# Kernel optimization log

Hardware: AMD Instinct MI355X
Metric: run time of the kernel (lower is better)

Reference implementation:

```python
import jax, jax.numpy as jnp
import numpy as np

B = 1000        # graphs in batch
T_PER = 250     # tasks per graph
M_PER = 50      # machines per graph
N_T = B * T_PER
N_M = B * M_PER
D_T = 16        # INPUT_TASK_DIM
D_M = 8         # INPUT_MACHINE_DIM
H = 128         # hidden_dim
IN_PREV_IDX = 0
TASK_FEAT_IDX = 1
EPS = 1e-5      # BatchNorm eps


def _mk_params(rng):
    def lin(i, o):
        return (rng.standard_normal((i, o)).astype(np.float32) / np.sqrt(i),
                np.zeros(o, np.float32))
    p = {}
    p['bn_t_gamma'] = np.ones(D_T, np.float32); p['bn_t_beta'] = np.zeros(D_T, np.float32)
    p['Wt1'], p['bt1'] = lin(D_T, H); p['Wt2'], p['bt2'] = lin(H, H)
    p['bn_m_gamma'] = np.ones(D_M, np.float32); p['bn_m_beta'] = np.zeros(D_M, np.float32)
    p['Wm1'], p['bm1'] = lin(D_M, H); p['Wm2'], p['bm2'] = lin(H, H)
    p['Wa1'], p['ba1'] = lin(2 * H, H); p['Wa2'], p['ba2'] = lin(H, H)
    p['Wl1'], p['bl1'] = lin(3 * H, H); p['Wl2'], p['bl2'] = lin(H, H)
    p['Wo1'], p['bo1'] = lin(H, H); p['Wo2'], p['bo2'] = lin(H, 1)
    return p


def setup_inputs() -> dict:
    rng = np.random.default_rng(0)
    xt = rng.standard_normal((N_T, D_T)).astype(np.float32)
    # prev-task flag: even task ids are 'prev'
    xt[:, IN_PREV_IDX] = (np.arange(N_T) % 2 == 0).astype(np.float32)
    # per-graph machine assignment in [0, M_PER), or -1 (unassigned) every 10th task
    lm = rng.integers(0, M_PER, N_T)
    lm[np.arange(N_T) % 10 == 0] = -1
    xt[:, TASK_FEAT_IDX] = lm.astype(np.float32)
    xm = rng.standard_normal((N_M, D_M)).astype(np.float32)
    inp = {'x_tasks': jnp.asarray(xt), 'x_machines': jnp.asarray(xm)}
    inp.update({k: jnp.asarray(v) for k, v in _mk_params(rng).items()})
    inp['x_tasks_batch'] = jnp.asarray(np.repeat(np.arange(B), T_PER).astype(np.int32))
    inp['x_machines_batch'] = jnp.asarray(np.repeat(np.arange(B), M_PER).astype(np.int32))
    # labels are tasks 0,5,10,...; prev tasks are even ids -> prev-local index t//2
    # label tasks that are prev: t % 10 == 0 -> prev_tasks_label_idx = 5*arange(N_T//10)
    inp['label_idx'] = jnp.asarray((5 * np.arange(N_T // 10)).astype(np.int32))
    inp['num_graphs'] = B
    return inp


def _bn(x, g, b):
    # BatchNorm1d in training mode: biased batch stats
    mu = x.mean(axis=0)
    var = x.var(axis=0)
    return g * (x - mu) * jax.lax.rsqrt(var + EPS) + b


def _seg_mean(x, seg, n):
    s = jax.ops.segment_sum(x, seg, num_segments=n)
    c = jax.ops.segment_sum(jnp.ones((x.shape[0], 1), x.dtype), seg, num_segments=n)
    return s / jnp.maximum(c, 1.0)


def reference(x_tasks, x_machines, bn_t_gamma, bn_t_beta, Wt1, bt1, Wt2, bt2,
              bn_m_gamma, bn_m_beta, Wm1, bm1, Wm2, bm2,
              Wa1, ba1, Wa2, ba2, Wl1, bl1, Wl2, bl2,
              Wo1, bo1, Wo2, bo2,
              x_tasks_batch, x_machines_batch, label_idx, num_graphs):
    nm = x_machines.shape[0]
    # tasks_select_assignment: local machine id -> global machine row (or pad row nm)
    tm_col = x_tasks[:, TASK_FEAT_IDX]
    cnt_m = jnp.bincount(x_machines_batch, length=num_graphs)
    cum = jnp.cumsum(cnt_m) - cnt_m  # cumulative machines per graph
    task_m = jnp.where(tm_col == -1.0, nm,
                       tm_col.astype(jnp.int32) + cum[x_tasks_batch].astype(jnp.int32))
    # node embeddings: BN -> Linear -> ReLU -> Linear -> ReLU
    th = jax.nn.relu(jax.nn.relu(_bn(x_tasks, bn_t_gamma, bn_t_beta) @ Wt1 + bt1) @ Wt2 + bt2)
    mh = jax.nn.relu(jax.nn.relu(_bn(x_machines, bn_m_gamma, bn_m_beta) @ Wm1 + bm1) @ Wm2 + bm2)
    # global aggregation per graph (scatter_mean) + MLP
    aggr = jnp.concatenate([_seg_mean(th, x_tasks_batch, num_graphs),
                            _seg_mean(mh, x_machines_batch, num_graphs)], axis=1)
    aggr = jax.nn.relu(aggr @ Wa1 + ba1) @ Wa2 + ba2
    # gather machine embedding per task (pad row of zeros for unassigned)
    mh_pad = jnp.concatenate([mh, jnp.zeros((1, H), mh.dtype)], axis=0)
    cat = jnp.concatenate([th, aggr[x_tasks_batch], mh_pad[task_m]], axis=1)  # [N_T, 3H]
    h = jax.nn.relu(cat @ Wl1 + bl1) @ Wl2 + bl2
    out = (jax.nn.relu(h @ Wo1 + bo1) @ Wo2 + bo2)[label_idx]
    return out
```

## Files before the change

### kernel.cpp

```cpp
#include <hip/hip_runtime.h>
#include <hip/hip_bf16.h>

constexpr int B     = 1000;
constexpr int T_PER = 250;
constexpr int M_PER = 50;
constexpr int N_T   = B * T_PER;
constexpr int N_M   = B * M_PER;
constexpr int H     = 128;
constexpr int N_LBL = 25000;
constexpr float EPS = 1e-05f;

constexpr int NB_T = 256;
constexpr int NB_M = 64;
constexpr int NB_P = 64;

constexpr int OFF_PART_T = 0;
constexpr int OFF_PART_M = OFF_PART_T + NB_T * 32;
constexpr int OFF_AT     = OFF_PART_M + NB_M * 16;
constexpr int OFF_BT     = OFF_AT + 16;
constexpr int OFF_AM     = OFF_BT + 16;
constexpr int OFF_BM     = OFF_AM + 8;
constexpr int OFF_BT1F   = OFF_BM + 8;
constexpr int OFF_BM1F   = OFF_BT1F + 128;
constexpr int OFF_MEANT  = OFF_BM1F + 128;
constexpr int OFF_MEANM  = OFF_MEANT + B * H;
constexpr int OFF_HALF   = OFF_MEANM + B * H;
constexpr int HO_WT1  = 0;
constexpr int HO_WT2  = 4096;
constexpr int HO_WM1  = 20480;
constexpr int HO_WM2  = 24576;
constexpr int HO_WA1  = 40960;
constexpr int HO_WA2  = 73728;
constexpr int HO_WL1  = 90112;
constexpr int HO_WL2  = 139264;
constexpr int HO_WO1  = 155648;

typedef _Float16 f16x8 __attribute__((ext_vector_type(8)));
typedef _Float16 f16x4 __attribute__((ext_vector_type(4)));
typedef float f32x4 __attribute__((ext_vector_type(4)));

#define MFMA16(a, b, c) __builtin_amdgcn_mfma_f32_16x16x32_f16(a, b, c, 0, 0, 0)

template <int C, int NB>
__device__ __forceinline__ void stats_body(const float* __restrict__ x, int nelem,
                                           float* __restrict__ part, int blk, int t,
                                           float* ls, float* lq) {
    float s = 0.f, q = 0.f;
    for (int e = blk * 256 + t; e < nelem; e += NB * 256) {
        float v = x[e];
        s += v;
        q += v * v;
    }
    ls[t] = s; lq[t] = q;
    __syncthreads();
    if (t < C) {
        float S = 0.f, Q = 0.f;
        for (int u = t; u < 256; u += C) { S += ls[u]; Q += lq[u]; }
        part[blk * 2 * C + t] = S;
        part[blk * 2 * C + C + t] = Q;
    }
}

__device__ __forceinline__ void cvt_tr(const float* __restrict__ src, _Float16* __restrict__ dst,
                                       int K, int Kp, int tid, int nt) {
    for (int idx = tid; idx < 128 * Kp; idx += nt) {
        int c = idx / Kp, k = idx - c * Kp;
        float v = (k < K) ? src[k * 128 + c] : 0.f;
        dst[idx] = (_Float16)v;
    }
}

__global__ __launch_bounds__(256) void stats_prep_kernel(
        const float* __restrict__ xt, const float* __restrict__ xm,
        const float* __restrict__ Wt1, const float* __restrict__ Wt2,
        const float* __restrict__ Wm1, const float* __restrict__ Wm2,
        const float* __restrict__ Wa1, const float* __restrict__ Wa2,
        const float* __restrict__ Wl1, const float* __restrict__ Wl2,
        const float* __restrict__ Wo1,
        float* __restrict__ wsf, _Float16* __restrict__ wh) {
    __shared__ float ls[256], lq[256];
    const int bid = blockIdx.x, t = threadIdx.x;
    if (bid < NB_T) {
        stats_body<16, NB_T>(xt, N_T * 16, wsf + OFF_PART_T, bid, t, ls, lq);
    } else if (bid < NB_T + NB_M) {
        stats_body<8, NB_M>(xm, N_M * 8, wsf + OFF_PART_M, bid - NB_T, t, ls, lq);
    } else {
        const int tid = (bid - NB_T - NB_M) * 256 + t;
        const int nt = NB_P * 256;
        cvt_tr(Wt1, wh + HO_WT1, 16, 32, tid, nt);
        cvt_tr(Wt2, wh + HO_WT2, 128, 128, tid, nt);
        cvt_tr(Wm1, wh + HO_WM1, 8, 32, tid, nt);
        cvt_tr(Wm2, wh + HO_WM2, 128, 128, tid, nt);
        cvt_tr(Wa1, wh + HO_WA1, 256, 256, tid, nt);
        cvt_tr(Wa2, wh + HO_WA2, 128, 128, tid, nt);
        cvt_tr(Wl1, wh + HO_WL1, 384, 384, tid, nt);
        cvt_tr(Wl2, wh + HO_WL2, 128, 128, tid, nt);
        cvt_tr(Wo1, wh + HO_WO1, 128, 128, tid, nt);
    }
}

__global__ __launch_bounds__(256) void finalize_kernel(
        const float* __restrict__ gt, const float* __restrict__ btb,
        const float* __restrict__ gm, const float* __restrict__ bmb,
        const float* __restrict__ Wt1, const float* __restrict__ bt1,
        const float* __restrict__ Wm1, const float* __restrict__ bm1,
        float* __restrict__ ws) {
    __shared__ float red[256];
    __shared__ float statT[32], statM[16];
    __shared__ float shT[16], shM[8];
    const int t = threadIdx.x;
    {
        const int slot = t & 31, chunk = t >> 5;
        const float* p = ws + OFF_PART_T;
        float s = 0.f;
        for (int b = chunk * 32; b < chunk * 32 + 32; b++) s += p[b * 32 + slot];
        red[t] = s;
    }
    __syncthreads();
    if (t < 32) {
        float v = 0.f;
#pragma unroll
        for (int c = 0; c < 8; c++) v += red[t + 32 * c];
        statT[t] = v;
    }
    __syncthreads();
    {
        float s = 0.f;
        if (t < 128) {
            const int slot = t & 15, chunk = t >> 4;
            const float* p = ws + OFF_PART_M;
            for (int b = chunk * 8; b < chunk * 8 + 8; b++) s += p[b * 16 + slot];
        }
        red[t] = s;
    }
    __syncthreads();
    if (t < 16) {
        float v = 0.f;
#pragma unroll
        for (int c = 0; c < 8; c++) v += red[t + 16 * c];
        statM[t] = v;
    }
    __syncthreads();
    if (t < 16) {
        float mu  = statT[t] / (float)N_T;
        float var = statT[16 + t] / (float)N_T - mu * mu;
        float a   = gt[t] * rsqrtf(var + EPS);
        ws[OFF_AT + t] = a;
        float b = btb[t] - mu * a;
        ws[OFF_BT + t] = b;
        shT[t] = b;
    } else if (t < 24) {
        int c = t - 16;
        float mu  = statM[c] / (float)N_M;
        float var = statM[8 + c] / (float)N_M - mu * mu;
        float a   = gm[c] * rsqrtf(var + EPS);
        ws[OFF_AM + c] = a;
        float b = bmb[c] - mu * a;
        ws[OFF_BM + c] = b;
        shM[c] = b;
    }
    __syncthreads();
    if (t < 128) {
        float s = bt1[t];
#pragma unroll
        for (int k = 0; k < 16; k++) s += shT[k] * Wt1[k * 128 + t];
        ws[OFF_BT1F + t] = s;
    } else {
        int c = t - 128;
        float s = bm1[c];
#pragma unroll
        for (int k = 0; k < 8; k++) s += shM[k] * Wm1[k * 128 + c];
        ws[OFF_BM1F + c] = s;
    }
}

__device__ __forceinline__ void zacc(f32x4 acc[4][2]) {
#pragma unroll
    for (int rg = 0; rg < 4; rg++)
#pragma unroll
        for (int mi = 0; mi < 2; mi++) acc[rg][mi] = (f32x4){0.f, 0.f, 0.f, 0.f};
}

__device__ __forceinline__ void ld32(f16x8 w[2], const _Float16* __restrict__ WT,
                                     int m0, int r, int gq) {
#pragma unroll
    for (int mi = 0; mi < 2; mi++)
        w[mi] = *(const f16x8*)(WT + ((m0 + mi) * 16 + r) * 32 + gq * 8);
}

__device__ __forceinline__ void ld128(f16x8 w[2][4], const _Float16* __restrict__ WT,
                                      int lda, int k0, int m0, int r, int gq) {
#pragma unroll
    for (int mi = 0; mi < 2; mi++)
#pragma unroll
        for (int ks = 0; ks < 4; ks++)
            w[mi][ks] = *(const f16x8*)(WT + ((m0 + mi) * 16 + r) * lda + k0 + ks * 32 + gq * 8);
}

__device__ __forceinline__ void mm32(const f16x8 w[2], const _Float16* __restrict__ act,
                                     int rstride, int r, int gq, f32x4 acc[4][2]) {
#pragma unroll
    for (int rg = 0; rg < 4; rg++) {
        const f16x8 bf = *(const f16x8*)(act + (rg * 16 + r) * rstride + gq * 8);
        acc[rg][0] = MFMA16(w[0], bf, acc[rg][0]);
        acc[rg][1] = MFMA16(w[1], bf, acc[rg][1]);
    }
}

__device__ __forceinline__ void mm128(const f16x8 w[2][4], const _Float16* __restrict__ act,
                                      int rstride, int r, int gq, f32x4 acc[4][2]) {
#pragma unroll
    for (int rg = 0; rg < 4; rg++)
#pragma unroll
        for (int ks = 0; ks < 4; ks++) {
            const f16x8 bf = *(const f16x8*)(act + (rg * 16 + r) * rstride + ks * 32 + gq * 8);
            acc[rg][0] = MFMA16(w[0][ks], bf, acc[rg][0]);
            acc[rg][1] = MFMA16(w[1][ks], bf, acc[rg][1]);
        }
}

__device__ __forceinline__ void epi_cs(const f32x4 acc[4][2], const f32x4 bv[2],
                                       _Float16* __restrict__ dst, int dstride,
                                       int m0, int r, int gq, bool relu) {
#pragma unroll
    for (int rg = 0; rg < 4; rg++)
#pragma unroll
        for (int mi = 0; mi < 2; mi++) {
            f16x4 hv;
#pragma unroll
            for (int j = 0; j < 4; j++) {
                float v = acc[rg][mi][j] + bv[mi][j];
                if (relu) v = fmaxf(v, 0.f);
                hv[j] = (_Float16)v;
            }
            *(f16x4*)(dst + (rg * 16 + r) * dstride + (m0 + mi) * 16 + gq * 4) = hv;
        }
}

template <int CIN, int ROWS, int PASSES>
__device__ __forceinline__ void seg_body(const float* __restrict__ x, const float* __restrict__ scaleA,
        const _Float16* __restrict__ W1T, const float* __restrict__ b1,
        const _Float16* __restrict__ W2T, const float* __restrict__ b2,
        float* __restrict__ meanout, int g, int t,
        _Float16* __restrict__ xs, _Float16* __restrict__ h1s) {
    const int lane = t & 63, wave = t >> 6;
    const int r = lane & 15, gq = lane >> 4;
    const int m0 = 2 * wave;
    f16x8 w1[2], w2[2][4];
    ld32(w1, W1T, m0, r, gq);
    ld128(w2, W2T, 128, 0, m0, r, gq);
    f32x4 b1v[2], b2v[2];
#pragma unroll
    for (int mi = 0; mi < 2; mi++) {
        b1v[mi] = *(const f32x4*)(b1 + (m0 + mi) * 16 + gq * 4);
        b2v[mi] = *(const f32x4*)(b2 + (m0 + mi) * 16 + gq * 4);
    }
    const int jrow = (CIN == 16) ? (t >> 2) : (t >> 1);
    const int part = (CIN == 16) ? (t & 3) : (t & 1);
    const bool stager = (CIN == 16) ? true : (t < 128);
    f32x4 av = {0.f, 0.f, 0.f, 0.f};
    if (stager) av = *(const f32x4*)(scaleA + part * 4);
    f16x4 z4; z4[0] = z4[1] = z4[2] = z4[3] = (_Float16)0.f;
    if (stager) {
        if (CIN == 16) {
            *(f16x4*)(xs + jrow * 40 + 16 + part * 4) = z4;
        } else {
#pragma unroll
            for (int q = 0; q < 3; q++)
                *(f16x4*)(xs + jrow * 40 + 8 + part * 12 + q * 4) = z4;
        }
    }
    float4 xr = {0.f, 0.f, 0.f, 0.f};
    if (stager) {
        int cl = (jrow < ROWS) ? jrow : (ROWS - 1);
        xr = *(const float4*)(x + (g * ROWS + cl) * CIN + part * 4);
    }
    f32x4 rs[2];
    rs[0] = (f32x4){0.f, 0.f, 0.f, 0.f};
    rs[1] = (f32x4){0.f, 0.f, 0.f, 0.f};
    for (int p = 0; p < PASSES; p++) {
        if (stager) {
            const bool valid = (p * 64 + jrow) < ROWS;
            f16x4 hv;
            hv[0] = (_Float16)(valid ? av[0] * xr.x : 0.f);
            hv[1] = (_Float16)(valid ? av[1] * xr.y : 0.f);
            hv[2] = (_Float16)(valid ? av[2] * xr.z : 0.f);
            hv[3] = (_Float16)(valid ? av[3] * xr.w : 0.f);
            *(f16x4*)(xs + jrow * 40 + part * 4) = hv;
        }
        __syncthreads();
        if (p + 1 < PASSES && stager) {
            int lr = (p + 1) * 64 + jrow;
            int cl = (lr < ROWS) ? lr : (ROWS - 1);
            xr = *(const float4*)(x + (g * ROWS + cl) * CIN + part * 4);
        }
        f32x4 acc[4][2];
        zacc(acc);
        mm32(w1, xs, 40, r, gq, acc);
        epi_cs(acc, b1v, h1s, 136, m0, r, gq, true);
        __syncthreads();
        zacc(acc);
        mm128(w2, h1s, 136, r, gq, acc);
#pragma unroll
        for (int rg = 0; rg < 4; rg++) {
            const bool vr = (p * 64 + rg * 16 + r) < ROWS;
#pragma unroll
            for (int mi = 0; mi < 2; mi++)
#pragma unroll
                for (int j = 0; j < 4; j++) {
                    float v = fmaxf(acc[rg][mi][j] + b2v[mi][j], 0.f);
                    rs[mi][j] += vr ? v : 0.f;
                }
        }
    }
#pragma unroll
    for (int mi = 0; mi < 2; mi++)
#pragma unroll
        for (int j = 0; j < 4; j++) {
            float v = rs[mi][j];
            v += __shfl_xor(v, 1); v += __shfl_xor(v, 2);
            v += __shfl_xor(v, 4); v += __shfl_xor(v, 8);
            rs[mi][j] = v;
        }
    if (r == 0) {
        constexpr float inv = 1.f / (float)ROWS;
#pragma unroll
        for (int mi = 0; mi < 2; mi++) {
            f32x4 st = rs[mi] * inv;
            *(f32x4*)(meanout + g * H + (m0 + mi) * 16 + gq * 4) = st;
        }
    }
}

__global__ __launch_bounds__(256) void seg_fused(const float* __restrict__ xt, const float* __restrict__ xm,
        const _Float16* __restrict__ wh, const float* __restrict__ wsf,
        const float* __restrict__ bt2, const float* __restrict__ bm2,
        float* __restrict__ meanT, float* __restrict__ meanM) {
    __shared__ __attribute__((aligned(16))) _Float16 xs[64 * 40];
    __shared__ __attribute__((aligned(16))) _Float16 h1s[64 * 136];
    if (blockIdx.x < B)
        seg_body<16, T_PER, 4>(xt, wsf + OFF_AT, wh + HO_WT1, wsf + OFF_BT1F,
                               wh + HO_WT2, bt2, meanT, blockIdx.x, threadIdx.x, xs, h1s);
    else
        seg_body<8, M_PER, 1>(xm, wsf + OFF_AM, wh + HO_WM1, wsf + OFF_BM1F,
                              wh + HO_WM2, bm2, meanM, blockIdx.x - B, threadIdx.x, xs, h1s);
}

__global__ __launch_bounds__(256) void aggr_kernel(const float* __restrict__ meanT, const float* __restrict__ meanM,
        const _Float16* __restrict__ Wa1T, const float* __restrict__ ba1,
        const _Float16* __restrict__ Wa2T, const float* __restrict__ ba2,
        const _Float16* __restrict__ Wl1T, const float* __restrict__ bl1,
        float* __restrict__ agg2) {
    __shared__ __attribute__((aligned(16))) _Float16 cin[16 * 264];
    __shared__ __attribute__((aligned(16))) _Float16 h1s[16 * 136];
    __shared__ __attribute__((aligned(16))) _Float16 ags[16 * 136];
    const int t = threadIdx.x, lane = t & 63, wave = t >> 6;
    const int r = lane & 15, gq = lane >> 4;
    const int m0 = 2 * wave;
    const int g0 = blockIdx.x * 16;
    f16x8 wa1[2][8], wa2[2][4], wl1b[2][4];
#pragma unroll
    for (int mi = 0; mi < 2; mi++)
#pragma unroll
        for (int ks = 0; ks < 8; ks++)
            wa1[mi][ks] = *(const f16x8*)(Wa1T + ((m0 + mi) * 16 + r) * 256 + ks * 32 + gq * 8);
    ld128(wa2, Wa2T, 128, 0, m0, r, gq);
    ld128(wl1b, Wl1T, 384, 128, m0, r, gq);
    f32x4 b1v[2], b2v[2], blv[2];
#pragma unroll
    for (int mi = 0; mi < 2; mi++) {
        b1v[mi] = *(const f32x4*)(ba1 + (m0 + mi) * 16 + gq * 4);
        b2v[mi] = *(const f32x4*)(ba2 + (m0 + mi) * 16 + gq * 4);
        blv[mi] = *(const f32x4*)(bl1 + (m0 + mi) * 16 + gq * 4);
    }
    for (int e = t; e < 16 * 64; e += 256) {
        int j = e >> 6, c4 = e & 63;
        int g = g0 + j;
        float4 v = {0.f, 0.f, 0.f, 0.f};
        if (g < B) v = (c4 < 32) ? *(const float4*)(meanT + g * H + c4 * 4)
                                 : *(const float4*)(meanM + g * H + (c4 - 32) * 4);
        f16x4 hv;
        hv[0] = (_Float16)v.x; hv[1] = (_Float16)v.y; hv[2] = (_Float16)v.z; hv[3] = (_Float16)v.w;
        *(f16x4*)(cin + j * 264 + c4 * 4) = hv;
    }
    __syncthreads();
    f32x4 a0 = {0.f, 0.f, 0.f, 0.f}, a1 = {0.f, 0.f, 0.f, 0.f};
    {
        const _Float16* bp = cin + r * 264 + gq * 8;
#pragma unroll
        for (int ks = 0; ks < 8; ks++) {
            const f16x8 bf = *(const f16x8*)(bp + ks * 32);
            a0 = MFMA16(wa1[0][ks], bf, a0);
            a1 = MFMA16(wa1[1][ks], bf, a1);
        }
    }
    {
        f16x4 h0, h1v;
#pragma unroll
        for (int j = 0; j < 4; j++) {
            h0[j]  = (_Float16)fmaxf(a0[j] + b1v[0][j], 0.f);
            h1v[j] = (_Float16)fmaxf(a1[j] + b1v[1][j], 0.f);
        }
        *(f16x4*)(h1s + r * 136 + m0 * 16 + gq * 4) = h0;
        *(f16x4*)(h1s + r * 136 + (m0 + 1) * 16 + gq * 4) = h1v;
    }
    __syncthreads();
    a0 = (f32x4){0.f, 0.f, 0.f, 0.f}; a1 = (f32x4){0.f, 0.f, 0.f, 0.f};
    {
        const _Float16* bp = h1s + r * 136 + gq * 8;
#pragma unroll
        for (int ks = 0; ks < 4; ks++) {
            const f16x8 bf = *(const f16x8*)(bp + ks * 32);
            a0 = MFMA16(wa2[0][ks], bf, a0);
            a1 = MFMA16(wa2[1][ks], bf, a1);
        }
    }
    {
        f16x4 h0, h1v;
#pragma unroll
        for (int j = 0; j < 4; j++) {
            h0[j]  = (_Float16)(a0[j] + b2v[0][j]);
            h1v[j] = (_Float16)(a1[j] + b2v[1][j]);
        }
        *(f16x4*)(ags + r * 136 + m0 * 16 + gq * 4) = h0;
        *(f16x4*)(ags + r * 136 + (m0 + 1) * 16 + gq * 4) = h1v;
    }
    __syncthreads();
    a0 = (f32x4){0.f, 0.f, 0.f, 0.f}; a1 = (f32x4){0.f, 0.f, 0.f, 0.f};
    {
        const _Float16* bp = ags + r * 136 + gq * 8;
#pragma unroll
        for (int ks = 0; ks < 4; ks++) {
            const f16x8 bf = *(const f16x8*)(bp + ks * 32);
            a0 = MFMA16(wl1b[0][ks], bf, a0);
            a1 = MFMA16(wl1b[1][ks], bf, a1);
        }
    }
    if (g0 + r < B) {
        *(f32x4*)(agg2 + (g0 + r) * H + m0 * 16 + gq * 4) = a0 + blv[0];
        *(f32x4*)(agg2 + (g0 + r) * H + (m0 + 1) * 16 + gq * 4) = a1 + blv[1];
    }
}

__global__ __launch_bounds__(256) void label_kernel(
        const float* __restrict__ xt, const float* __restrict__ xm,
        const float* __restrict__ scT, const float* __restrict__ scM,
        const _Float16* __restrict__ Wt1T, const float* __restrict__ bt1f,
        const _Float16* __restrict__ Wt2T, const float* __restrict__ bt2,
        const _Float16* __restrict__ Wm1T, const float* __restrict__ bm1f,
        const _Float16* __restrict__ Wm2T, const float* __restrict__ bm2,
        const _Float16* __restrict__ Wl1T,
        const _Float16* __restrict__ Wl2T, const float* __restrict__ bl2,
        const _Float16* __restrict__ Wo1T, const float* __restrict__ bo1,
        const float* __restrict__ Wo2, const float* __restrict__ bo2,
        const float* __restrict__ agg2,
        const int* __restrict__ tbatch, const int* __restrict__ lidx,
        float* __restrict__ out) {
    __shared__ __attribute__((aligned(16))) _Float16 xs_t[64 * 40];
    __shared__ __attribute__((aligned(16))) _Float16 xs_m[64 * 40];
    __shared__ __attribute__((aligned(16))) _Float16 h1s[64 * 136];
    __shared__ __attribute__((aligned(16))) _Float16 cat[64 * 264];
    __shared__ float psum[4][64];
    __shared__ int ridx[64], gidx[64], midx[64];
    const int t = threadIdx.x;
    const int lane = t & 63, wave = t >> 6;
    const int r = lane & 15, gq = lane >> 4;
    const int m0 = 2 * wave;
    if (t < 64) {
        int i = blockIdx.x * 64 + t;
        int rr = (i < N_LBL) ? lidx[i] : 0;
        ridx[t] = rr;
        int gg = tbatch[rr];
        gidx[t] = gg;
        float tv = xt[rr * 16 + 1];
        midx[t] = (tv == -1.0f) ? -1 : ((int)tv + gg * M_PER);
    }
    __syncthreads();
    f16x4 z4; z4[0] = z4[1] = z4[2] = z4[3] = (_Float16)0.f;
    {
        int j = t >> 2, part = t & 3;
        f32x4 avt = *(const f32x4*)(scT + part * 4);
        float4 v = *(const float4*)(xt + ridx[j] * 16 + part * 4);
        f16x4 hv;
        hv[0] = (_Float16)(avt[0] * v.x); hv[1] = (_Float16)(avt[1] * v.y);
        hv[2] = (_Float16)(avt[2] * v.z); hv[3] = (_Float16)(avt[3] * v.w);
        *(f16x4*)(xs_t + j * 40 + part * 4) = hv;
        *(f16x4*)(xs_t + j * 40 + 16 + part * 4) = z4;
    }
    if (t < 128) {
        int j = t >> 1, part = t & 1;
        f32x4 avm = *(const f32x4*)(scM + part * 4);
        int m = midx[j];
        f16x4 hv = z4;
        if (m >= 0) {
            float4 v = *(const float4*)(xm + m * 8 + part * 4);
            hv[0] = (_Float16)(avm[0] * v.x); hv[1] = (_Float16)(avm[1] * v.y);
            hv[2] = (_Float16)(avm[2] * v.z); hv[3] = (_Float16)(avm[3] * v.w);
        }
        *(f16x4*)(xs_m + j * 40 + part * 4) = hv;
#pragma unroll
        for (int q = 0; q < 3; q++)
            *(f16x4*)(xs_m + j * 40 + 8 + part * 12 + q * 4) = z4;
    }
    __syncthreads();
    f32x4 agg2v[4][2];
#pragma unroll
    for (int rg = 0; rg < 4; rg++)
#pragma unroll
        for (int mi = 0; mi < 2; mi++)
            agg2v[rg][mi] = *(const f32x4*)(agg2 + gidx[rg * 16 + r] * H + (m0 + mi) * 16 + gq * 4);
    f32x4 acc[4][2];
    f16x8 wt1[2]; ld32(wt1, Wt1T, m0, r, gq);
    f16x8 wt2[2][4]; ld128(wt2, Wt2T, 128, 0, m0, r, gq);
    f32x4 bva[2], bvb[2];
#pragma unroll
    for (int mi = 0; mi < 2; mi++) {
        bva[mi] = *(const f32x4*)(bt1f + (m0 + mi) * 16 + gq * 4);
        bvb[mi] = *(const f32x4*)(bt2 + (m0 + mi) * 16 + gq * 4);
    }
    zacc(acc);
    mm32(wt1, xs_t, 40, r, gq, acc);
    epi_cs(acc, bva, h1s, 136, m0, r, gq, true);
    f16x8 wm1[2]; ld32(wm1, Wm1T, m0, r, gq);
    __syncthreads();
    zacc(acc);
    mm128(wt2, h1s, 136, r, gq, acc);
    epi_cs(acc, bvb, cat, 264, m0, r, gq, true);
    f16x8 wm2[2][4]; ld128(wm2, Wm2T, 128, 0, m0, r, gq);
    __syncthreads();
#pragma unroll
    for (int mi = 0; mi < 2; mi++) {
        bva[mi] = *(const f32x4*)(bm1f + (m0 + mi) * 16 + gq * 4);
        bvb[mi] = *(const f32x4*)(bm2 + (m0 + mi) * 16 + gq * 4);
    }
    zacc(acc);
    mm32(wm1, xs_m, 40, r, gq, acc);
    epi_cs(acc, bva, h1s, 136, m0, r, gq, true);
    f16x8 wl1a[2][4]; ld128(wl1a, Wl1T, 384, 0, m0, r, gq);
    __syncthreads();
    zacc(acc);
    mm128(wm2, h1s, 136, r, gq, acc);
#pragma unroll
    for (int rg = 0; rg < 4; rg++) {
        const bool sent = (midx[rg * 16 + r] < 0);
#pragma unroll
        for (int mi = 0; mi < 2; mi++) {
            f16x4 hv;
#pragma unroll
            for (int j = 0; j < 4; j++) {
                float v = fmaxf(acc[rg][mi][j] + bvb[mi][j], 0.f);
                hv[j] = (_Float16)(sent ? 0.f : v);
            }
            *(f16x4*)(cat + (rg * 16 + r) * 264 + 128 + (m0 + mi) * 16 + gq * 4) = hv;
        }
    }
    f16x8 wl1c[2][4]; ld128(wl1c, Wl1T, 384, 256, m0, r, gq);
    __syncthreads();
    zacc(acc);
    mm128(wl1a, cat, 264, r, gq, acc);
    mm128(wl1c, cat + 128, 264, r, gq, acc);
#pragma unroll
    for (int rg = 0; rg < 4; rg++)
#pragma unroll
        for (int mi = 0; mi < 2; mi++) {
            f16x4 hv;
#pragma unroll
            for (int j = 0; j < 4; j++)
                hv[j] = (_Float16)fmaxf(acc[rg][mi][j] + agg2v[rg][mi][j], 0.f);
            *(f16x4*)(h1s + (rg * 16 + r) * 136 + (m0 + mi) * 16 + gq * 4) = hv;
        }
    f16x8 wl2[2][4]; ld128(wl2, Wl2T, 128, 0, m0, r, gq);
    __syncthreads();
#pragma unroll
    for (int mi = 0; mi < 2; mi++) bva[mi] = *(const f32x4*)(bl2 + (m0 + mi) * 16 + gq * 4);
    zacc(acc);
    mm128(wl2, h1s, 136, r, gq, acc);
    epi_cs(acc, bva, cat, 264, m0, r, gq, false);
    f16x8 wo1[2][4]; ld128(wo1, Wo1T, 128, 0, m0, r, gq);
    __syncthreads();
#pragma unroll
    for (int mi = 0; mi < 2; mi++) bva[mi] = *(const f32x4*)(bo1 + (m0 + mi) * 16 + gq * 4);
    f32x4 wo2v[2];
#pragma unroll
    for (int mi = 0; mi < 2; mi++) wo2v[mi] = *(const f32x4*)(Wo2 + (m0 + mi) * 16 + gq * 4);
    zacc(acc);
    mm128(wo1, cat, 264, r, gq, acc);
#pragma unroll
    for (int rg = 0; rg < 4; rg++) {
        float pv = 0.f;
#pragma unroll
        for (int mi = 0; mi < 2; mi++)
#pragma unroll
            for (int j = 0; j < 4; j++)
                pv += fmaxf(acc[rg][mi][j] + bva[mi][j], 0.f) * wo2v[mi][j];
        pv += __shfl_xor(pv, 16);
        pv += __shfl_xor(pv, 32);
        if (lane < 16) psum[wave][rg * 16 + lane] = pv;
    }
    __syncthreads();
    if (t < 64) {
        int i = blockIdx.x * 64 + t;
        if (i < N_LBL)
            out[i] = psum[0][t] + psum[1][t] + psum[2][t] + psum[3][t] + bo2[0];
    }
}

extern "C" void kernel_launch(void* const* d_in, const int* in_sizes, int n_in,
                              void* d_out, int out_size, void* d_ws, size_t ws_size,
                              hipStream_t stream) {
    const float* xt  = (const float*)d_in[0];
    const float* xm  = (const float*)d_in[1];
    const float* gt  = (const float*)d_in[2];
    const float* btb = (const float*)d_in[3];
    const float* Wt1 = (const float*)d_in[4];  const float* bt1 = (const float*)d_in[5];
    const float* Wt2 = (const float*)d_in[6];  const float* bt2 = (const float*)d_in[7];
    const float* gm  = (const float*)d_in[8];  const float* bmb = (const float*)d_in[9];
    const float* Wm1 = (const float*)d_in[10]; const float* bm1 = (const float*)d_in[11];
    const float* Wm2 = (const float*)d_in[12]; const float* bm2 = (const float*)d_in[13];
    const float* Wa1 = (const float*)d_in[14]; const float* ba1 = (const float*)d_in[15];
    const float* Wa2 = (const float*)d_in[16]; const float* ba2 = (const float*)d_in[17];
    const float* Wl1 = (const float*)d_in[18]; const float* bl1 = (const float*)d_in[19];
    const float* Wl2 = (const float*)d_in[20]; const float* bl2 = (const float*)d_in[21];
    const float* Wo1 = (const float*)d_in[22]; const float* bo1 = (const float*)d_in[23];
    const float* Wo2 = (const float*)d_in[24]; const float* bo2 = (const float*)d_in[25];
    const int* tb  = (const int*)d_in[26];
    const int* lix = (const int*)d_in[28];
    float* wsf = (float*)d_ws;
    _Float16* wh = (_Float16*)(wsf + OFF_HALF);
    float* outp = (float*)d_out;

    stats_prep_kernel<<<NB_T + NB_M + NB_P, 256, 0, stream>>>(
        xt, xm, Wt1, Wt2, Wm1, Wm2, Wa1, Wa2, Wl1, Wl2, Wo1, wsf, wh);
    finalize_kernel<<<1, 256, 0, stream>>>(gt, btb, gm, bmb, Wt1, bt1, Wm1, bm1, wsf);
    seg_fused<<<2 * B, 256, 0, stream>>>(xt, xm, wh, wsf, bt2, bm2,
                                         wsf + OFF_MEANT, wsf + OFF_MEANM);
    aggr_kernel<<<(B + 15) / 16, 256, 0, stream>>>(wsf + OFF_MEANT, wsf + OFF_MEANM,
                                                   wh + HO_WA1, ba1, wh + HO_WA2, ba2,
                                                   wh + HO_WL1, bl1, wsf + OFF_MEANT);
    label_kernel<<<(N_LBL + 63) / 64, 256, 0, stream>>>(xt, xm,
                                                        wsf + OFF_AT, wsf + OFF_AM,
                                                        wh + HO_WT1, wsf + OFF_BT1F, wh + HO_WT2, bt2,
                                                        wh + HO_WM1, wsf + OFF_BM1F, wh + HO_WM2, bm2,
                                                        wh + HO_WL1,
                                                        wh + HO_WL2, bl2,
                                                        wh + HO_WO1, bo1, Wo2, bo2,
                                                        wsf + OFF_MEANT, tb, lix, outp);
}
```

Measured before the change: 74.12 us.

## Fuse BN finalize and aggregation MLP into consumers, stage inputs as fp16

Removes the single-block finalize kernel and the aggr kernel. Each seg and label block now recomputes the BatchNorm statistics from the partial sums and folds the scale into the first-layer weights. The label kernel computes the per-graph aggregation MLP for the graphs it touches in shared memory. The stats pass also writes fp16 copies of the task and machine inputs so later kernels read half the bytes. This cuts two launches and their serialization, at the cost of redundant per-block reductions and MLP work, plus an extra fp16 write in the stats pass.

```diff
diff --git a/kernel.cpp b/kernel.cpp
--- a/kernel.cpp
+++ b/kernel.cpp
@@ -1,5 +1,4 @@
 #include <hip/hip_runtime.h>
-#include <hip/hip_bf16.h>
 
 constexpr int B     = 1000;
 constexpr int T_PER = 250;
@@ -16,13 +15,7 @@
 
 constexpr int OFF_PART_T = 0;
 constexpr int OFF_PART_M = OFF_PART_T + NB_T * 32;
-constexpr int OFF_AT     = OFF_PART_M + NB_M * 16;
-constexpr int OFF_BT     = OFF_AT + 16;
-constexpr int OFF_AM     = OFF_BT + 16;
-constexpr int OFF_BM     = OFF_AM + 8;
-constexpr int OFF_BT1F   = OFF_BM + 8;
-constexpr int OFF_BM1F   = OFF_BT1F + 128;
-constexpr int OFF_MEANT  = OFF_BM1F + 128;
+constexpr int OFF_MEANT  = OFF_PART_M + NB_M * 16;
 constexpr int OFF_MEANM  = OFF_MEANT + B * H;
 constexpr int OFF_HALF   = OFF_MEANM + B * H;
 constexpr int HO_WT1  = 0;
@@ -34,6 +27,8 @@
 constexpr int HO_WL1  = 90112;
 constexpr int HO_WL2  = 139264;
 constexpr int HO_WO1  = 155648;
+constexpr int HO_XT16 = 172032;
+constexpr int HO_XM16 = HO_XT16 + N_T * 16;
 
 typedef _Float16 f16x8 __attribute__((ext_vector_type(8)));
 typedef _Float16 f16x4 __attribute__((ext_vector_type(4)));
@@ -42,7 +37,8 @@
 #define MFMA16(a, b, c) __builtin_amdgcn_mfma_f32_16x16x32_f16(a, b, c, 0, 0, 0)
 
 template <int C, int NB>
-__device__ __forceinline__ void stats_body(const float* __restrict__ x, int nelem,
+__device__ __forceinline__ void stats_body(const float* __restrict__ x,
+                                           _Float16* __restrict__ x16, int nelem,
                                            float* __restrict__ part, int blk, int t,
                                            float* ls, float* lq) {
     float s = 0.f, q = 0.f;
@@ -50,6 +46,7 @@
         float v = x[e];
         s += v;
         q += v * v;
+        x16[e] = (_Float16)v;
     }
     ls[t] = s; lq[t] = q;
     __syncthreads();
@@ -72,6 +69,7 @@
 
 __global__ __launch_bounds__(256) void stats_prep_kernel(
         const float* __restrict__ xt, const float* __restrict__ xm,
+        _Float16* __restrict__ xt16, _Float16* __restrict__ xm16,
         const float* __restrict__ Wt1, const float* __restrict__ Wt2,
         const float* __restrict__ Wm1, const float* __restrict__ Wm2,
         const float* __restrict__ Wa1, const float* __restrict__ Wa2,
@@ -81,9 +79,9 @@
     __shared__ float ls[256], lq[256];
     const int bid = blockIdx.x, t = threadIdx.x;
     if (bid < NB_T) {
-        stats_body<16, NB_T>(xt, N_T * 16, wsf + OFF_PART_T, bid, t, ls, lq);
+        stats_body<16, NB_T>(xt, xt16, N_T * 16, wsf + OFF_PART_T, bid, t, ls, lq);
     } else if (bid < NB_T + NB_M) {
-        stats_body<8, NB_M>(xm, N_M * 8, wsf + OFF_PART_M, bid - NB_T, t, ls, lq);
+        stats_body<8, NB_M>(xm, xm16, N_M * 8, wsf + OFF_PART_M, bid - NB_T, t, ls, lq);
     } else {
         const int tid = (bid - NB_T - NB_M) * 256 + t;
         const int nt = NB_P * 256;
@@ -99,81 +97,6 @@
     }
 }
 
-__global__ __launch_bounds__(256) void finalize_kernel(
-        const float* __restrict__ gt, const float* __restrict__ btb,
-        const float* __restrict__ gm, const float* __restrict__ bmb,
-        const float* __restrict__ Wt1, const float* __restrict__ bt1,
-        const float* __restrict__ Wm1, const float* __restrict__ bm1,
-        float* __restrict__ ws) {
-    __shared__ float red[256];
-    __shared__ float statT[32], statM[16];
-    __shared__ float shT[16], shM[8];
-    const int t = threadIdx.x;
-    {
-        const int slot = t & 31, chunk = t >> 5;
-        const float* p = ws + OFF_PART_T;
-        float s = 0.f;
-        for (int b = chunk * 32; b < chunk * 32 + 32; b++) s += p[b * 32 + slot];
-        red[t] = s;
-    }
-    __syncthreads();
-    if (t < 32) {
-        float v = 0.f;
-#pragma unroll
-        for (int c = 0; c < 8; c++) v += red[t + 32 * c];
-        statT[t] = v;
-    }
-    __syncthreads();
-    {
-        float s = 0.f;
-        if (t < 128) {
-            const int slot = t & 15, chunk = t >> 4;
-            const float* p = ws + OFF_PART_M;
-            for (int b = chunk * 8; b < chunk * 8 + 8; b++) s += p[b * 16 + slot];
-        }
-        red[t] = s;
-    }
-    __syncthreads();
-    if (t < 16) {
-        float v = 0.f;
-#pragma unroll
-        for (int c = 0; c < 8; c++) v += red[t + 16 * c];
-        statM[t] = v;
-    }
-    __syncthreads();
-    if (t < 16) {
-        float mu  = statT[t] / (float)N_T;
-        float var = statT[16 + t] / (float)N_T - mu * mu;
-        float a   = gt[t] * rsqrtf(var + EPS);
-        ws[OFF_AT + t] = a;
-        float b = btb[t] - mu * a;
-        ws[OFF_BT + t] = b;
-        shT[t] = b;
-    } else if (t < 24) {
-        int c = t - 16;
-        float mu  = statM[c] / (float)N_M;
-        float var = statM[8 + c] / (float)N_M - mu * mu;
-        float a   = gm[c] * rsqrtf(var + EPS);
-        ws[OFF_AM + c] = a;
-        float b = bmb[c] - mu * a;
-        ws[OFF_BM + c] = b;
-        shM[c] = b;
-    }
-    __syncthreads();
-    if (t < 128) {
-        float s = bt1[t];
-#pragma unroll
-        for (int k = 0; k < 16; k++) s += shT[k] * Wt1[k * 128 + t];
-        ws[OFF_BT1F + t] = s;
-    } else {
-        int c = t - 128;
-        float s = bm1[c];
-#pragma unroll
-        for (int k = 0; k < 8; k++) s += shM[k] * Wm1[k * 128 + c];
-        ws[OFF_BM1F + c] = s;
-    }
-}
-
 __device__ __forceinline__ void zacc(f32x4 acc[4][2]) {
 #pragma unroll
     for (int rg = 0; rg < 4; rg++)
@@ -237,43 +160,85 @@
         }
 }
 
-template <int CIN, int ROWS, int PASSES>
-__device__ __forceinline__ void seg_body(const float* __restrict__ x, const float* __restrict__ scaleA,
-        const _Float16* __restrict__ W1T, const float* __restrict__ b1,
-        const _Float16* __restrict__ W2T, const float* __restrict__ b2,
-        float* __restrict__ meanout, int g, int t,
-        _Float16* __restrict__ xs, _Float16* __restrict__ h1s) {
+template <int CIN, int ROWS, int PASSES, int NBS, int NTOT>
+__device__ __forceinline__ void seg_body(
+        const _Float16* __restrict__ x16, const float* __restrict__ pstats,
+        const float* __restrict__ gamma, const float* __restrict__ beta,
+        const float* __restrict__ W1f, const float* __restrict__ b1,
+        const _Float16* __restrict__ W1T, const _Float16* __restrict__ W2T,
+        const float* __restrict__ b2, float* __restrict__ meanout,
+        int g, int t,
+        _Float16* __restrict__ xs, _Float16* __restrict__ h1s,
+        float* __restrict__ red, float* __restrict__ stat,
+        float* __restrict__ sa, float* __restrict__ sb, float* __restrict__ b1f) {
+    constexpr int S2 = 2 * CIN;
+    constexpr int NCH = 256 / S2;
+    {
+        const int slot = t & (S2 - 1), chunk = t / S2;
+        float s = 0.f;
+        for (int b = chunk; b < NBS; b += NCH) s += pstats[b * S2 + slot];
+        red[t] = s;
+    }
+    __syncthreads();
+    if (t < S2) {
+        float v = 0.f;
+#pragma unroll
+        for (int c = 0; c < NCH; c++) v += red[t + S2 * c];
+        stat[t] = v;
+    }
+    __syncthreads();
+    if (t < CIN) {
+        float mu  = stat[t] * (1.f / (float)NTOT);
+        float var = stat[CIN + t] * (1.f / (float)NTOT) - mu * mu;
+        float a   = gamma[t] * rsqrtf(var + EPS);
+        sa[t] = a;
+        sb[t] = beta[t] - mu * a;
+    }
+    __syncthreads();
+    if (t < 128) {
+        float s = b1[t];
+#pragma unroll
+        for (int k = 0; k < CIN; k++) s += sb[k] * W1f[k * 128 + t];
+        b1f[t] = s;
+    }
+    __syncthreads();
+
     const int lane = t & 63, wave = t >> 6;
     const int r = lane & 15, gq = lane >> 4;
     const int m0 = 2 * wave;
     f16x8 w1[2], w2[2][4];
     ld32(w1, W1T, m0, r, gq);
+    if (gq * 8 < CIN) {
+#pragma unroll
+        for (int mi = 0; mi < 2; mi++)
+#pragma unroll
+            for (int e = 0; e < 8; e++)
+                w1[mi][e] = (_Float16)((float)w1[mi][e] * sa[gq * 8 + e]);
+    }
     ld128(w2, W2T, 128, 0, m0, r, gq);
     f32x4 b1v[2], b2v[2];
 #pragma unroll
     for (int mi = 0; mi < 2; mi++) {
-        b1v[mi] = *(const f32x4*)(b1 + (m0 + mi) * 16 + gq * 4);
+        b1v[mi] = *(const f32x4*)(b1f + (m0 + mi) * 16 + gq * 4);
         b2v[mi] = *(const f32x4*)(b2 + (m0 + mi) * 16 + gq * 4);
     }
     const int jrow = (CIN == 16) ? (t >> 2) : (t >> 1);
-    const int part = (CIN == 16) ? (t & 3) : (t & 1);
+    const int prt  = (CIN == 16) ? (t & 3) : (t & 1);
     const bool stager = (CIN == 16) ? true : (t < 128);
-    f32x4 av = {0.f, 0.f, 0.f, 0.f};
-    if (stager) av = *(const f32x4*)(scaleA + part * 4);
     f16x4 z4; z4[0] = z4[1] = z4[2] = z4[3] = (_Float16)0.f;
     if (stager) {
         if (CIN == 16) {
-            *(f16x4*)(xs + jrow * 40 + 16 + part * 4) = z4;
+            *(f16x4*)(xs + jrow * 40 + 16 + prt * 4) = z4;
         } else {
 #pragma unroll
             for (int q = 0; q < 3; q++)
-                *(f16x4*)(xs + jrow * 40 + 8 + part * 12 + q * 4) = z4;
-        }
-    }
-    float4 xr = {0.f, 0.f, 0.f, 0.f};
+                *(f16x4*)(xs + jrow * 40 + 8 + prt * 12 + q * 4) = z4;
+        }
+    }
+    f16x4 xr = z4;
     if (stager) {
         int cl = (jrow < ROWS) ? jrow : (ROWS - 1);
-        xr = *(const float4*)(x + (g * ROWS + cl) * CIN + part * 4);
+        xr = *(const f16x4*)(x16 + (g * ROWS + cl) * CIN + prt * 4);
     }
     f32x4 rs[2];
     rs[0] = (f32x4){0.f, 0.f, 0.f, 0.f};
@@ -281,18 +246,14 @@
     for (int p = 0; p < PASSES; p++) {
         if (stager) {
             const bool valid = (p * 64 + jrow) < ROWS;
-            f16x4 hv;
-            hv[0] = (_Float16)(valid ? av[0] * xr.x : 0.f);
-            hv[1] = (_Float16)(valid ? av[1] * xr.y : 0.f);
-            hv[2] = (_Float16)(valid ? av[2] * xr.z : 0.f);
-            hv[3] = (_Float16)(valid ? av[3] * xr.w : 0.f);
-            *(f16x4*)(xs + jrow * 40 + part * 4) = hv;
+            f16x4 hv = valid ? xr : z4;
+            *(f16x4*)(xs + jrow * 40 + prt * 4) = hv;
         }
         __syncthreads();
         if (p + 1 < PASSES && stager) {
             int lr = (p + 1) * 64 + jrow;
             int cl = (lr < ROWS) ? lr : (ROWS - 1);
-            xr = *(const float4*)(x + (g * ROWS + cl) * CIN + part * 4);
+            xr = *(const f16x4*)(x16 + (g * ROWS + cl) * CIN + prt * 4);
         }
         f32x4 acc[4][2];
         zacc(acc);
@@ -301,16 +262,24 @@
         __syncthreads();
         zacc(acc);
         mm128(w2, h1s, 136, r, gq, acc);
-#pragma unroll
-        for (int rg = 0; rg < 4; rg++) {
-            const bool vr = (p * 64 + rg * 16 + r) < ROWS;
-#pragma unroll
-            for (int mi = 0; mi < 2; mi++)
-#pragma unroll
-                for (int j = 0; j < 4; j++) {
-                    float v = fmaxf(acc[rg][mi][j] + b2v[mi][j], 0.f);
-                    rs[mi][j] += vr ? v : 0.f;
-                }
+        if ((p + 1) * 64 <= ROWS) {
+#pragma unroll
+            for (int rg = 0; rg < 4; rg++)
+#pragma unroll
+                for (int mi = 0; mi < 2; mi++)
+#pragma unroll
+                    for (int j = 0; j < 4; j++)
+                        rs[mi][j] += fmaxf(acc[rg][mi][j] + b2v[mi][j], 0.f);
+        } else {
+#pragma unroll
+            for (int rg = 0; rg < 4; rg++) {
+                const float mk = ((p * 64 + rg * 16 + r) < ROWS) ? 1.f : 0.f;
+#pragma unroll
+                for (int mi = 0; mi < 2; mi++)
+#pragma unroll
+                    for (int j = 0; j < 4; j++)
+                        rs[mi][j] = fmaf(fmaxf(acc[rg][mi][j] + b2v[mi][j], 0.f), mk, rs[mi][j]);
+            }
         }
     }
 #pragma unroll
@@ -332,128 +301,42 @@
     }
 }
 
-__global__ __launch_bounds__(256) void seg_fused(const float* __restrict__ xt, const float* __restrict__ xm,
-        const _Float16* __restrict__ wh, const float* __restrict__ wsf,
+__global__ __launch_bounds__(256) void seg_fused(
+        const _Float16* __restrict__ xt16, const _Float16* __restrict__ xm16,
+        const float* __restrict__ wsf,
+        const float* __restrict__ gt, const float* __restrict__ btb,
+        const float* __restrict__ gm, const float* __restrict__ bmb,
+        const float* __restrict__ Wt1f, const float* __restrict__ bt1,
+        const float* __restrict__ Wm1f, const float* __restrict__ bm1,
+        const _Float16* __restrict__ wh,
         const float* __restrict__ bt2, const float* __restrict__ bm2,
         float* __restrict__ meanT, float* __restrict__ meanM) {
     __shared__ __attribute__((aligned(16))) _Float16 xs[64 * 40];
     __shared__ __attribute__((aligned(16))) _Float16 h1s[64 * 136];
+    __shared__ float red[256], stat[32], sa[16], sb[16], b1f[128];
     if (blockIdx.x < B)
-        seg_body<16, T_PER, 4>(xt, wsf + OFF_AT, wh + HO_WT1, wsf + OFF_BT1F,
-                               wh + HO_WT2, bt2, meanT, blockIdx.x, threadIdx.x, xs, h1s);
+        seg_body<16, T_PER, 4, NB_T, N_T>(xt16, wsf + OFF_PART_T, gt, btb, Wt1f, bt1,
+                                          wh + HO_WT1, wh + HO_WT2, bt2, meanT,
+                                          blockIdx.x, threadIdx.x, xs, h1s, red, stat, sa, sb, b1f);
     else
-        seg_body<8, M_PER, 1>(xm, wsf + OFF_AM, wh + HO_WM1, wsf + OFF_BM1F,
-                              wh + HO_WM2, bm2, meanM, blockIdx.x - B, threadIdx.x, xs, h1s);
-}
-
-__global__ __launch_bounds__(256) void aggr_kernel(const float* __restrict__ meanT, const float* __restrict__ meanM,
-        const _Float16* __restrict__ Wa1T, const float* __restrict__ ba1,
-        const _Float16* __restrict__ Wa2T, const float* __restrict__ ba2,
-        const _Float16* __restrict__ Wl1T, const float* __restrict__ bl1,
-        float* __restrict__ agg2) {
-    __shared__ __attribute__((aligned(16))) _Float16 cin[16 * 264];
-    __shared__ __attribute__((aligned(16))) _Float16 h1s[16 * 136];
-    __shared__ __attribute__((aligned(16))) _Float16 ags[16 * 136];
-    const int t = threadIdx.x, lane = t & 63, wave = t >> 6;
-    const int r = lane & 15, gq = lane >> 4;
-    const int m0 = 2 * wave;
-    const int g0 = blockIdx.x * 16;
-    f16x8 wa1[2][8], wa2[2][4], wl1b[2][4];
-#pragma unroll
-    for (int mi = 0; mi < 2; mi++)
-#pragma unroll
-        for (int ks = 0; ks < 8; ks++)
-            wa1[mi][ks] = *(const f16x8*)(Wa1T + ((m0 + mi) * 16 + r) * 256 + ks * 32 + gq * 8);
-    ld128(wa2, Wa2T, 128, 0, m0, r, gq);
-    ld128(wl1b, Wl1T, 384, 128, m0, r, gq);
-    f32x4 b1v[2], b2v[2], blv[2];
-#pragma unroll
-    for (int mi = 0; mi < 2; mi++) {
-        b1v[mi] = *(const f32x4*)(ba1 + (m0 + mi) * 16 + gq * 4);
-        b2v[mi] = *(const f32x4*)(ba2 + (m0 + mi) * 16 + gq * 4);
-        blv[mi] = *(const f32x4*)(bl1 + (m0 + mi) * 16 + gq * 4);
-    }
-    for (int e = t; e < 16 * 64; e += 256) {
-        int j = e >> 6, c4 = e & 63;
-        int g = g0 + j;
-        float4 v = {0.f, 0.f, 0.f, 0.f};
-        if (g < B) v = (c4 < 32) ? *(const float4*)(meanT + g * H + c4 * 4)
-                                 : *(const float4*)(meanM + g * H + (c4 - 32) * 4);
-        f16x4 hv;
-        hv[0] = (_Float16)v.x; hv[1] = (_Float16)v.y; hv[2] = (_Float16)v.z; hv[3] = (_Float16)v.w;
-        *(f16x4*)(cin + j * 264 + c4 * 4) = hv;
-    }
-    __syncthreads();
-    f32x4 a0 = {0.f, 0.f, 0.f, 0.f}, a1 = {0.f, 0.f, 0.f, 0.f};
-    {
-        const _Float16* bp = cin + r * 264 + gq * 8;
-#pragma unroll
-        for (int ks = 0; ks < 8; ks++) {
-            const f16x8 bf = *(const f16x8*)(bp + ks * 32);
-            a0 = MFMA16(wa1[0][ks], bf, a0);
-            a1 = MFMA16(wa1[1][ks], bf, a1);
-        }
-    }
-    {
-        f16x4 h0, h1v;
-#pragma unroll
-        for (int j = 0; j < 4; j++) {
-            h0[j]  = (_Float16)fmaxf(a0[j] + b1v[0][j], 0.f);
-            h1v[j] = (_Float16)fmaxf(a1[j] + b1v[1][j], 0.f);
-        }
-        *(f16x4*)(h1s + r * 136 + m0 * 16 + gq * 4) = h0;
-        *(f16x4*)(h1s + r * 136 + (m0 + 1) * 16 + gq * 4) = h1v;
-    }
-    __syncthreads();
-    a0 = (f32x4){0.f, 0.f, 0.f, 0.f}; a1 = (f32x4){0.f, 0.f, 0.f, 0.f};
-    {
-        const _Float16* bp = h1s + r * 136 + gq * 8;
-#pragma unroll
-        for (int ks = 0; ks < 4; ks++) {
-            const f16x8 bf = *(const f16x8*)(bp + ks * 32);
-            a0 = MFMA16(wa2[0][ks], bf, a0);
-            a1 = MFMA16(wa2[1][ks], bf, a1);
-        }
-    }
-    {
-        f16x4 h0, h1v;
-#pragma unroll
-        for (int j = 0; j < 4; j++) {
-            h0[j]  = (_Float16)(a0[j] + b2v[0][j]);
-            h1v[j] = (_Float16)(a1[j] + b2v[1][j]);
-        }
-        *(f16x4*)(ags + r * 136 + m0 * 16 + gq * 4) = h0;
-        *(f16x4*)(ags + r * 136 + (m0 + 1) * 16 + gq * 4) = h1v;
-    }
-    __syncthreads();
-    a0 = (f32x4){0.f, 0.f, 0.f, 0.f}; a1 = (f32x4){0.f, 0.f, 0.f, 0.f};
-    {
-        const _Float16* bp = ags + r * 136 + gq * 8;
-#pragma unroll
-        for (int ks = 0; ks < 4; ks++) {
-            const f16x8 bf = *(const f16x8*)(bp + ks * 32);
-            a0 = MFMA16(wl1b[0][ks], bf, a0);
-            a1 = MFMA16(wl1b[1][ks], bf, a1);
-        }
-    }
-    if (g0 + r < B) {
-        *(f32x4*)(agg2 + (g0 + r) * H + m0 * 16 + gq * 4) = a0 + blv[0];
-        *(f32x4*)(agg2 + (g0 + r) * H + (m0 + 1) * 16 + gq * 4) = a1 + blv[1];
-    }
+        seg_body<8, M_PER, 1, NB_M, N_M>(xm16, wsf + OFF_PART_M, gm, bmb, Wm1f, bm1,
+                                         wh + HO_WM1, wh + HO_WM2, bm2, meanM,
+                                         blockIdx.x - B, threadIdx.x, xs, h1s, red, stat, sa, sb, b1f);
 }
 
 __global__ __launch_bounds__(256) void label_kernel(
-        const float* __restrict__ xt, const float* __restrict__ xm,
-        const float* __restrict__ scT, const float* __restrict__ scM,
-        const _Float16* __restrict__ Wt1T, const float* __restrict__ bt1f,
-        const _Float16* __restrict__ Wt2T, const float* __restrict__ bt2,
-        const _Float16* __restrict__ Wm1T, const float* __restrict__ bm1f,
-        const _Float16* __restrict__ Wm2T, const float* __restrict__ bm2,
-        const _Float16* __restrict__ Wl1T,
-        const _Float16* __restrict__ Wl2T, const float* __restrict__ bl2,
-        const _Float16* __restrict__ Wo1T, const float* __restrict__ bo1,
+        const float* __restrict__ xt,
+        const _Float16* __restrict__ xt16, const _Float16* __restrict__ xm16,
+        const float* __restrict__ wsf, const _Float16* __restrict__ wh,
+        const float* __restrict__ gt, const float* __restrict__ btb,
+        const float* __restrict__ gm, const float* __restrict__ bmb,
+        const float* __restrict__ Wt1f, const float* __restrict__ bt1,
+        const float* __restrict__ Wm1f, const float* __restrict__ bm1,
+        const float* __restrict__ bt2, const float* __restrict__ bm2,
+        const float* __restrict__ ba1, const float* __restrict__ ba2,
+        const float* __restrict__ bl1, const float* __restrict__ bl2,
+        const float* __restrict__ bo1,
         const float* __restrict__ Wo2, const float* __restrict__ bo2,
-        const float* __restrict__ agg2,
         const int* __restrict__ tbatch, const int* __restrict__ lidx,
         float* __restrict__ out) {
     __shared__ __attribute__((aligned(16))) _Float16 xs_t[64 * 40];
@@ -461,11 +344,19 @@
     __shared__ __attribute__((aligned(16))) _Float16 h1s[64 * 136];
     __shared__ __attribute__((aligned(16))) _Float16 cat[64 * 264];
     __shared__ float psum[4][64];
-    __shared__ int ridx[64], gidx[64], midx[64];
+    __shared__ int ridx[64], gidx[64], midx[64], slotS[64];
+    __shared__ float red[256], statT[32], statM[16];
+    __shared__ float saT[16], sbT[16], saM[8], sbM[8];
+    __shared__ float b1ft[128], b1fm[128];
+    __shared__ __attribute__((aligned(16))) float agg2s[16 * 132];
+
+    const float* meanT = wsf + OFF_MEANT;
+    const float* meanM = wsf + OFF_MEANM;
     const int t = threadIdx.x;
     const int lane = t & 63, wave = t >> 6;
     const int r = lane & 15, gq = lane >> 4;
     const int m0 = 2 * wave;
+
     if (t < 64) {
         int i = blockIdx.x * 64 + t;
         int rr = (i < N_LBL) ? lidx[i] : 0;
@@ -475,68 +366,214 @@
         float tv = xt[rr * 16 + 1];
         midx[t] = (tv == -1.0f) ? -1 : ((int)tv + gg * M_PER);
     }
-    __syncthreads();
+    {
+        const int slot = t & 31, chunk = t >> 5;
+        const float* p = wsf + OFF_PART_T;
+        float s = 0.f;
+        for (int b = chunk; b < NB_T; b += 8) s += p[b * 32 + slot];
+        red[t] = s;
+    }
+    __syncthreads();
+    const int gbase = gidx[0];
+    if (t < 32) {
+        float v = 0.f;
+#pragma unroll
+        for (int c = 0; c < 8; c++) v += red[t + 32 * c];
+        statT[t] = v;
+    }
+    if (t < 64) {
+        int sl = gidx[t] - gbase;
+        slotS[t] = (sl < 0) ? 0 : ((sl > 15) ? 15 : sl);
+    }
+    __syncthreads();
+    {
+        float s = 0.f;
+        if (t < 128) {
+            const int slot = t & 15, chunk = t >> 4;
+            const float* p = wsf + OFF_PART_M;
+            for (int b = chunk; b < NB_M; b += 8) s += p[b * 16 + slot];
+        }
+        red[t] = s;
+    }
+    __syncthreads();
+    if (t < 16) {
+        float v = 0.f;
+#pragma unroll
+        for (int c = 0; c < 8; c++) v += red[t + 16 * c];
+        statM[t] = v;
+    }
+    __syncthreads();
+    if (t < 16) {
+        float mu  = statT[t] * (1.f / (float)N_T);
+        float var = statT[16 + t] * (1.f / (float)N_T) - mu * mu;
+        float a   = gt[t] * rsqrtf(var + EPS);
+        saT[t] = a;
+        sbT[t] = btb[t] - mu * a;
+    } else if (t < 24) {
+        int c = t - 16;
+        float mu  = statM[c] * (1.f / (float)N_M);
+        float var = statM[8 + c] * (1.f / (float)N_M) - mu * mu;
+        float a   = gm[c] * rsqrtf(var + EPS);
+        saM[c] = a;
+        sbM[c] = bmb[c] - mu * a;
+    }
+    __syncthreads();
+    if (t < 128) {
+        float s = bt1[t];
+#pragma unroll
+        for (int k = 0; k < 16; k++) s += sbT[k] * Wt1f[k * 128 + t];
+        b1ft[t] = s;
+    } else {
+        int c = t - 128;
+        float s = bm1[c];
+#pragma unroll
+        for (int k = 0; k < 8; k++) s += sbM[k] * Wm1f[k * 128 + c];
+        b1fm[c] = s;
+    }
+    __syncthreads();
+
     f16x4 z4; z4[0] = z4[1] = z4[2] = z4[3] = (_Float16)0.f;
     {
-        int j = t >> 2, part = t & 3;
-        f32x4 avt = *(const f32x4*)(scT + part * 4);
-        float4 v = *(const float4*)(xt + ridx[j] * 16 + part * 4);
-        f16x4 hv;
-        hv[0] = (_Float16)(avt[0] * v.x); hv[1] = (_Float16)(avt[1] * v.y);
-        hv[2] = (_Float16)(avt[2] * v.z); hv[3] = (_Float16)(avt[3] * v.w);
-        *(f16x4*)(xs_t + j * 40 + part * 4) = hv;
-        *(f16x4*)(xs_t + j * 40 + 16 + part * 4) = z4;
+        int j = t >> 2, prt = t & 3;
+        f16x4 hv = *(const f16x4*)(xt16 + ridx[j] * 16 + prt * 4);
+        *(f16x4*)(xs_t + j * 40 + prt * 4) = hv;
+        *(f16x4*)(xs_t + j * 40 + 16 + prt * 4) = z4;
     }
     if (t < 128) {
-        int j = t >> 1, part = t & 1;
-        f32x4 avm = *(const f32x4*)(scM + part * 4);
+        int j = t >> 1, prt = t & 1;
         int m = midx[j];
         f16x4 hv = z4;
-        if (m >= 0) {
-            float4 v = *(const float4*)(xm + m * 8 + part * 4);
-            hv[0] = (_Float16)(avm[0] * v.x); hv[1] = (_Float16)(avm[1] * v.y);
-            hv[2] = (_Float16)(avm[2] * v.z); hv[3] = (_Float16)(avm[3] * v.w);
-        }
-        *(f16x4*)(xs_m + j * 40 + part * 4) = hv;
+        if (m >= 0) hv = *(const f16x4*)(xm16 + m * 8 + prt * 4);
+        *(f16x4*)(xs_m + j * 40 + prt * 4) = hv;
 #pragma unroll
         for (int q = 0; q < 3; q++)
-            *(f16x4*)(xs_m + j * 40 + 8 + part * 12 + q * 4) = z4;
-    }
-    __syncthreads();
-    f32x4 agg2v[4][2];
-#pragma unroll
-    for (int rg = 0; rg < 4; rg++)
+            *(f16x4*)(xs_m + j * 40 + 8 + prt * 12 + q * 4) = z4;
+    }
+    _Float16* cin = cat;
+    for (int e = t; e < 16 * 64; e += 256) {
+        int j = e >> 6, c4 = e & 63;
+        int g = gbase + j;
+        float4 v = {0.f, 0.f, 0.f, 0.f};
+        if (g < B) v = (c4 < 32) ? *(const float4*)(meanT + g * H + c4 * 4)
+                                 : *(const float4*)(meanM + g * H + (c4 - 32) * 4);
+        f16x4 hv;
+        hv[0] = (_Float16)v.x; hv[1] = (_Float16)v.y; hv[2] = (_Float16)v.z; hv[3] = (_Float16)v.w;
+        *(f16x4*)(cin + j * 264 + c4 * 4) = hv;
+    }
+    f16x8 wa1[2][8], wa2[2][4], wl1b[2][4];
+#pragma unroll
+    for (int mi = 0; mi < 2; mi++)
+#pragma unroll
+        for (int ks = 0; ks < 8; ks++)
+            wa1[mi][ks] = *(const f16x8*)(wh + HO_WA1 + ((m0 + mi) * 16 + r) * 256 + ks * 32 + gq * 8);
+    ld128(wa2, wh + HO_WA2, 128, 0, m0, r, gq);
+    ld128(wl1b, wh + HO_WL1, 384, 128, m0, r, gq);
+    f32x4 bav[2], bbv[2], blv2[2];
+#pragma unroll
+    for (int mi = 0; mi < 2; mi++) {
+        bav[mi]  = *(const f32x4*)(ba1 + (m0 + mi) * 16 + gq * 4);
+        bbv[mi]  = *(const f32x4*)(ba2 + (m0 + mi) * 16 + gq * 4);
+        blv2[mi] = *(const f32x4*)(bl1 + (m0 + mi) * 16 + gq * 4);
+    }
+    __syncthreads();
+    f32x4 a0 = {0.f, 0.f, 0.f, 0.f}, a1 = {0.f, 0.f, 0.f, 0.f};
+    {
+        const _Float16* bp = cin + r * 264 + gq * 8;
+#pragma unroll
+        for (int ks = 0; ks < 8; ks++) {
+            const f16x8 bf = *(const f16x8*)(bp + ks * 32);
+            a0 = MFMA16(wa1[0][ks], bf, a0);
+            a1 = MFMA16(wa1[1][ks], bf, a1);
+        }
+    }
+    {
+        f16x4 h0, h1v;
+#pragma unroll
+        for (int j = 0; j < 4; j++) {
+            h0[j]  = (_Float16)fmaxf(a0[j] + bav[0][j], 0.f);
+            h1v[j] = (_Float16)fmaxf(a1[j] + bav[1][j], 0.f);
+        }
+        *(f16x4*)(h1s + r * 136 + m0 * 16 + gq * 4) = h0;
+        *(f16x4*)(h1s + r * 136 + (m0 + 1) * 16 + gq * 4) = h1v;
+    }
+    __syncthreads();
+    a0 = (f32x4){0.f, 0.f, 0.f, 0.f}; a1 = (f32x4){0.f, 0.f, 0.f, 0.f};
+    {
+        const _Float16* bp = h1s + r * 136 + gq * 8;
+#pragma unroll
+        for (int ks = 0; ks < 4; ks++) {
+            const f16x8 bf = *(const f16x8*)(bp + ks * 32);
+            a0 = MFMA16(wa2[0][ks], bf, a0);
+            a1 = MFMA16(wa2[1][ks], bf, a1);
+        }
+    }
+    {
+        f16x4 h0, h1v;
+#pragma unroll
+        for (int j = 0; j < 4; j++) {
+            h0[j]  = (_Float16)(a0[j] + bbv[0][j]);
+            h1v[j] = (_Float16)(a1[j] + bbv[1][j]);
+        }
+        *(f16x4*)(cat + r * 136 + m0 * 16 + gq * 4) = h0;
+        *(f16x4*)(cat + r * 136 + (m0 + 1) * 16 + gq * 4) = h1v;
+    }
+    __syncthreads();
+    a0 = (f32x4){0.f, 0.f, 0.f, 0.f}; a1 = (f32x4){0.f, 0.f, 0.f, 0.f};
+    {
+        const _Float16* bp = cat + r * 136 + gq * 8;
+#pragma unroll
+        for (int ks = 0; ks < 4; ks++) {
+            const f16x8 bf = *(const f16x8*)(bp + ks * 32);
+            a0 = MFMA16(wl1b[0][ks], bf, a0);
+            a1 = MFMA16(wl1b[1][ks], bf, a1);
+        }
+    }
+    *(f32x4*)(agg2s + r * 132 + m0 * 16 + gq * 4) = a0 + blv2[0];
+    *(f32x4*)(agg2s + r * 132 + (m0 + 1) * 16 + gq * 4) = a1 + blv2[1];
+    __syncthreads();
+
+    f32x4 acc[4][2];
+    f16x8 wt1[2]; ld32(wt1, wh + HO_WT1, m0, r, gq);
+    if (gq < 2) {
 #pragma unroll
         for (int mi = 0; mi < 2; mi++)
-            agg2v[rg][mi] = *(const f32x4*)(agg2 + gidx[rg * 16 + r] * H + (m0 + mi) * 16 + gq * 4);
-    f32x4 acc[4][2];
-    f16x8 wt1[2]; ld32(wt1, Wt1T, m0, r, gq);
-    f16x8 wt2[2][4]; ld128(wt2, Wt2T, 128, 0, m0, r, gq);
+#pragma unroll
+            for (int e = 0; e < 8; e++)
+                wt1[mi][e] = (_Float16)((float)wt1[mi][e] * saT[gq * 8 + e]);
+    }
+    f16x8 wt2[2][4]; ld128(wt2, wh + HO_WT2, 128, 0, m0, r, gq);
     f32x4 bva[2], bvb[2];
 #pragma unroll
     for (int mi = 0; mi < 2; mi++) {
-        bva[mi] = *(const f32x4*)(bt1f + (m0 + mi) * 16 + gq * 4);
+        bva[mi] = *(const f32x4*)(b1ft + (m0 + mi) * 16 + gq * 4);
         bvb[mi] = *(const f32x4*)(bt2 + (m0 + mi) * 16 + gq * 4);
     }
     zacc(acc);
     mm32(wt1, xs_t, 40, r, gq, acc);
     epi_cs(acc, bva, h1s, 136, m0, r, gq, true);
-    f16x8 wm1[2]; ld32(wm1, Wm1T, m0, r, gq);
+    f16x8 wm1[2]; ld32(wm1, wh + HO_WM1, m0, r, gq);
+    if (gq == 0) {
+#pragma unroll
+        for (int mi = 0; mi < 2; mi++)
+#pragma unroll
+            for (int e = 0; e < 8; e++)
+                wm1[mi][e] = (_Float16)((float)wm1[mi][e] * saM[e]);
+    }
     __syncthreads();
     zacc(acc);
     mm128(wt2, h1s, 136, r, gq, acc);
     epi_cs(acc, bvb, cat, 264, m0, r, gq, true);
-    f16x8 wm2[2][4]; ld128(wm2, Wm2T, 128, 0, m0, r, gq);
+    f16x8 wm2[2][4]; ld128(wm2, wh + HO_WM2, 128, 0, m0, r, gq);
     __syncthreads();
 #pragma unroll
     for (int mi = 0; mi < 2; mi++) {
-        bva[mi] = *(const f32x4*)(bm1f + (m0 + mi) * 16 + gq * 4);
+        bva[mi] = *(const f32x4*)(b1fm + (m0 + mi) * 16 + gq * 4);
         bvb[mi] = *(const f32x4*)(bm2 + (m0 + mi) * 16 + gq * 4);
     }
     zacc(acc);
     mm32(wm1, xs_m, 40, r, gq, acc);
     epi_cs(acc, bva, h1s, 136, m0, r, gq, true);
-    f16x8 wl1a[2][4]; ld128(wl1a, Wl1T, 384, 0, m0, r, gq);
+    f16x8 wl1a[2][4]; ld128(wl1a, wh + HO_WL1, 384, 0, m0, r, gq);
     __syncthreads();
     zacc(acc);
     mm128(wm2, h1s, 136, r, gq, acc);
@@ -554,29 +591,32 @@
             *(f16x4*)(cat + (rg * 16 + r) * 264 + 128 + (m0 + mi) * 16 + gq * 4) = hv;
         }
     }
-    f16x8 wl1c[2][4]; ld128(wl1c, Wl1T, 384, 256, m0, r, gq);
+    f16x8 wl1c[2][4]; ld128(wl1c, wh + HO_WL1, 384, 256, m0, r, gq);
     __syncthreads();
     zacc(acc);
     mm128(wl1a, cat, 264, r, gq, acc);
     mm128(wl1c, cat + 128, 264, r, gq, acc);
 #pragma unroll
-    for (int rg = 0; rg < 4; rg++)
+    for (int rg = 0; rg < 4; rg++) {
+        const int sl = slotS[rg * 16 + r];
 #pragma unroll
         for (int mi = 0; mi < 2; mi++) {
+            f32x4 av2 = *(const f32x4*)(agg2s + sl * 132 + (m0 + mi) * 16 + gq * 4);
             f16x4 hv;
 #pragma unroll
             for (int j = 0; j < 4; j++)
-                hv[j] = (_Float16)fmaxf(acc[rg][mi][j] + agg2v[rg][mi][j], 0.f);
+                hv[j] = (_Float16)fmaxf(acc[rg][mi][j] + av2[j], 0.f);
             *(f16x4*)(h1s + (rg * 16 + r) * 136 + (m0 + mi) * 16 + gq * 4) = hv;
         }
-    f16x8 wl2[2][4]; ld128(wl2, Wl2T, 128, 0, m0, r, gq);
+    }
+    f16x8 wl2[2][4]; ld128(wl2, wh + HO_WL2, 128, 0, m0, r, gq);
     __syncthreads();
 #pragma unroll
     for (int mi = 0; mi < 2; mi++) bva[mi] = *(const f32x4*)(bl2 + (m0 + mi) * 16 + gq * 4);
     zacc(acc);
     mm128(wl2, h1s, 136, r, gq, acc);
     epi_cs(acc, bva, cat, 264, m0, r, gq, false);
-    f16x8 wo1[2][4]; ld128(wo1, Wo1T, 128, 0, m0, r, gq);
+    f16x8 wo1[2][4]; ld128(wo1, wh + HO_WO1, 128, 0, m0, r, gq);
     __syncthreads();
 #pragma unroll
     for (int mi = 0; mi < 2; mi++) bva[mi] = *(const f32x4*)(bo1 + (m0 + mi) * 16 + gq * 4);
@@ -627,22 +667,19 @@
     const int* lix = (const int*)d_in[28];
     float* wsf = (float*)d_ws;
     _Float16* wh = (_Float16*)(wsf + OFF_HALF);
+    _Float16* xt16 = wh + HO_XT16;
+    _Float16* xm16 = wh + HO_XM16;
     float* outp = (float*)d_out;
 
     stats_prep_kernel<<<NB_T + NB_M + NB_P, 256, 0, stream>>>(
-        xt, xm, Wt1, Wt2, Wm1, Wm2, Wa1, Wa2, Wl1, Wl2, Wo1, wsf, wh);
-    finalize_kernel<<<1, 256, 0, stream>>>(gt, btb, gm, bmb, Wt1, bt1, Wm1, bm1, wsf);
-    seg_fused<<<2 * B, 256, 0, stream>>>(xt, xm, wh, wsf, bt2, bm2,
+        xt, xm, xt16, xm16, Wt1, Wt2, Wm1, Wm2, Wa1, Wa2, Wl1, Wl2, Wo1, wsf, wh);
+    seg_fused<<<2 * B, 256, 0, stream>>>(xt16, xm16, wsf,
+                                         gt, btb, gm, bmb, Wt1, bt1, Wm1, bm1,
+                                         wh, bt2, bm2,
                                          wsf + OFF_MEANT, wsf + OFF_MEANM);
-    aggr_kernel<<<(B + 15) / 16, 256, 0, stream>>>(wsf + OFF_MEANT, wsf + OFF_MEANM,
-                                                   wh + HO_WA1, ba1, wh + HO_WA2, ba2,
-                                                   wh + HO_WL1, bl1, wsf + OFF_MEANT);
-    label_kernel<<<(N_LBL + 63) / 64, 256, 0, stream>>>(xt, xm,
-                                                        wsf + OFF_AT, wsf + OFF_AM,
-                                                        wh + HO_WT1, wsf + OFF_BT1F, wh + HO_WT2, bt2,
-                                                        wh + HO_WM1, wsf + OFF_BM1F, wh + HO_WM2, bm2,
-                                                        wh + HO_WL1,
-                                                        wh + HO_WL2, bl2,
-                                                        wh + HO_WO1, bo1, Wo2, bo2,
-                                                        wsf + OFF_MEANT, tb, lix, outp);
-}
+    label_kernel<<<(N_LBL + 63) / 64, 256, 0, stream>>>(xt, xt16, xm16, wsf, wh,
+                                                        gt, btb, gm, bmb,
+                                                        Wt1, bt1, Wm1, bm1,
+                                                        bt2, bm2, ba1, ba2, bl1, bl2, bo1,
+                                                        Wo2, bo2, tb, lix, outp);
+}
```

Result: slower. 92.21 us (+24.4%).
